# Kernel optimization log

Measured on AMD Instinct MI355X. Metric: run time of the kernel, lower is better.

The kernel has to match this reference:

```python
import jax, jax.numpy as jnp
import numpy as np


def _softsplat(tenIn, tenFlow):
    """Bilinear forward splatting: scatter tenIn to flow-displaced locations.
    tenIn: [N,C,H,W], tenFlow: [N,2,H,W] -> out [N,C,H,W]."""
    N, C, H, W = tenIn.shape
    dt = tenIn.dtype
    gx = jnp.arange(W, dtype=dt)[None, None, :]   # [1,1,W]
    gy = jnp.arange(H, dtype=dt)[None, :, None]   # [1,H,1]
    fx = gx + tenFlow[:, 0]                       # [N,H,W] target x
    fy = gy + tenFlow[:, 1]                       # [N,H,W] target y
    finite = jnp.isfinite(fx) & jnp.isfinite(fy)
    x0f = jnp.floor(fx)
    y0f = jnp.floor(fy)
    ix0 = x0f.astype(jnp.int32)
    iy0 = y0f.astype(jnp.int32)
    # bilinear corner weights (NW, NE, SW, SE) exactly as in the CUDA kernel
    wx1 = fx - x0f            # weight toward east
    wx0 = (x0f + 1.0) - fx    # weight toward west
    wy1 = fy - y0f            # weight toward south
    wy0 = (y0f + 1.0) - fy    # weight toward north
    corners = [
        (ix0,     iy0,     wx0 * wy0),  # NW
        (ix0 + 1, iy0,     wx1 * wy0),  # NE
        (ix0,     iy0 + 1, wx0 * wy1),  # SW
        (ix0 + 1, iy0 + 1, wx1 * wy1),  # SE
    ]
    HW = H * W
    tenIn_flat = tenIn.reshape(N, C, HW)

    def scatter_corner(ix, iy, w):
        valid = finite & (ix >= 0) & (ix < W) & (iy >= 0) & (iy < H)
        idx = jnp.where(valid, iy * W + ix, 0).reshape(N, HW)       # [N,HW]
        wv = jnp.where(valid, w, jnp.zeros_like(w)).reshape(N, 1, HW)
        vals = (tenIn_flat * wv).transpose(0, 2, 1)                 # [N,HW,C]
        seg = jax.vmap(lambda v, i: jax.ops.segment_sum(v, i, num_segments=HW))(vals, idx)
        return seg                                                   # [N,HW,C]

    out = scatter_corner(*corners[0])
    for c in corners[1:]:
        out = out + scatter_corner(*c)
    return out.transpose(0, 2, 1).reshape(N, C, H, W)


def softsplat_softmax(tenIn, tenFlow, tenMetric):
    # strMode == 'softmax': splat [tenIn * exp(metric), exp(metric)], then normalize
    w = jnp.exp(tenMetric)                          # [N,1,H,W]
    packed = jnp.concatenate([tenIn * w, w], axis=1)
    out = _softsplat(packed, tenFlow)
    norm = out[:, -1:]
    norm = jnp.where(norm == 0.0, jnp.ones_like(norm), norm)
    return out[:, :-1] / norm


def setup_inputs() -> dict:
    key = jax.random.key(0)
    k1, k2, k3 = jax.random.split(key, 3)
    N, C, H, W = 8, 64, 288, 512
    tenIn = jax.random.normal(k1, (N, C, H, W), dtype=jnp.float32)
    tenFlow = jax.random.normal(k2, (N, 2, H, W), dtype=jnp.float32)
    tenMetric = jax.random.normal(k3, (N, 1, H, W), dtype=jnp.float32)
    return {"tenIn": tenIn, "tenFlow": tenFlow, "tenMetric": tenMetric}


def reference(tenIn, tenFlow, tenMetric):
    return softsplat_softmax(tenIn, tenFlow, tenMetric)
```

## Files before the change

### kernel.cpp

```cpp
#include <hip/hip_runtime.h>
#include <hip/hip_fp16.h>
#include <math.h>

constexpr int N  = 8;
constexpr int C  = 64;
constexpr int H  = 288;
constexpr int W  = 512;
constexpr int HW = H * W;
constexpr int NPIX = N * HW;

constexpr int TW = 64, TH = 32, R = 8;
constexpr int PW = TW + 2 * R;
constexpr int PH = TH + 2 * R;
constexpr int PS = PW * PH;
constexpr int TGX = W / TW;
constexpr int TGY = H / TH;
constexpr int TILES = N * TGX * TGY;
constexpr int NOUT = TH * TW;
constexpr int K = 12;
constexpr int CCHB = 4;
constexpr int NCHUNK = C / CCHB;
constexpr int NSPLIT = 2;
constexpr int CPB = NCHUNK / NSPLIT;
constexpr int OVFCAP = 256;
constexpr int ESCCAP = 512;
constexpr int NTC = 512;
constexpr int NTG = 1024;
constexpr int GGRID = TILES * NSPLIT;

constexpr size_t CLAIM_LDS_WORDS = (size_t)NOUT * (K + 1);
constexpr size_t CLAIM_LDS_BYTES = CLAIM_LDS_WORDS * 4;

constexpr size_t WS_DEN  = 0;
constexpr size_t WS_META = WS_DEN  + (size_t)N * HW;
constexpr size_t WS_CNT  = WS_META + (size_t)TILES * NOUT * K;
constexpr size_t WS_OVFC = WS_CNT  + (size_t)TILES * NOUT;
constexpr size_t WS_OVFE = WS_OVFC + TILES;
constexpr size_t WS_ESCC = WS_OVFE + (size_t)TILES * OVFCAP * 2;
constexpr size_t WS_ESCE = WS_ESCC + TILES;

__device__ __forceinline__ int swz(int si) { return si ^ ((si >> 4) & 15); }

__device__ __forceinline__ unsigned packh2(float a, float b) {
    __half2 h = __floats2half2_rn(a, b);
    return *reinterpret_cast<unsigned*>(&h);
}
__device__ __forceinline__ float2 unpackh2(unsigned u) {
    __half2 h = *reinterpret_cast<__half2*>(&u);
    return __half22float2(h);
}

__global__ __launch_bounds__(NTC) void claim_kernel(
    const float* __restrict__ flow, const float* __restrict__ metric,
    unsigned* __restrict__ meta,
    unsigned* __restrict__ ovfc, unsigned* __restrict__ ovfe,
    float* __restrict__ den)
{
    extern __shared__ unsigned smem[];
    unsigned* cnt = smem;
    unsigned* ml  = smem + NOUT;

    for (int i = threadIdx.x; i < NOUT; i += NTC) cnt[i] = 0;
    for (int i = threadIdx.x; i < NOUT * K; i += NTC) ml[i] = 0u;
    __syncthreads();

    const int t  = blockIdx.x;
    const int n  = t / (TGX * TGY);
    const int r  = t % (TGX * TGY);
    const int Y0 = (r / TGX) * TH;
    const int X0 = (r % TGX) * TW;

    const float* fxp = flow + ((size_t)n * 2) * HW;
    const float* fyp = fxp + HW;
    const float* mp  = metric + (size_t)n * HW;
    unsigned* mt = meta + (size_t)t * NOUT * K;

    for (int si = threadIdx.x; si < PS; si += NTC) {
        int ys = Y0 - R + si / PW;
        int xs = X0 - R + si % PW;
        if ((unsigned)ys >= (unsigned)H || (unsigned)xs >= (unsigned)W) continue;
        int p = ys * W + xs;
        float fx = fxp[p] + (float)xs;
        float fy = fyp[p] + (float)ys;
        if (!(isfinite(fx) && isfinite(fy))) continue;
        float x0f = floorf(fx), y0f = floorf(fy);
        int tx = (int)x0f - X0;
        int ty = (int)y0f - Y0;
        float wx1 = fx - x0f, wx0 = x0f + 1.0f - fx;
        float wy1 = fy - y0f, wy0 = y0f + 1.0f - fy;
        float wm  = __expf(mp[p]);
        int sis = swz(si);

        #define CLAIM(TYv, TXv, Wv)                                           \
            if ((unsigned)(TYv) < (unsigned)TH &&                             \
                (unsigned)(TXv) < (unsigned)TW) {                             \
                float w_ = (Wv) * wm;                                         \
                int   o_ = (TYv) * TW + (TXv);                                \
                unsigned slot = atomicAdd(&cnt[o_], 1u);                      \
                if (slot < (unsigned)K) {                                     \
                    ml[o_ * K + (int)slot] =                                  \
                        ((unsigned)__half_as_ushort(__float2half(w_)) << 16)  \
                        | (unsigned)sis;                                      \
                } else {                                                      \
                    unsigned p2 = atomicAdd(&ovfc[t], 1u);                    \
                    if (p2 < (unsigned)OVFCAP) {                              \
                        unsigned* e = ovfe + ((size_t)t * OVFCAP + p2) * 2;   \
                        e[0] = ((unsigned)o_ << 16) | (unsigned)sis;          \
                        e[1] = __float_as_uint(w_);                           \
                    }                                                         \
                }                                                             \
            }
        CLAIM(ty,     tx,     wx0 * wy0)
        CLAIM(ty,     tx + 1, wx1 * wy0)
        CLAIM(ty + 1, tx,     wx0 * wy1)
        CLAIM(ty + 1, tx + 1, wx1 * wy1)
        #undef CLAIM
    }
    __syncthreads();

    const unsigned on = min(ovfc[t], (unsigned)OVFCAP);
    const unsigned* oe = ovfe + (size_t)t * OVFCAP * 2;
    for (int o = threadIdx.x; o < NOUT; o += NTC) {
        unsigned cn = min(cnt[o], (unsigned)K);
        float d = 0.0f;
        for (unsigned s = 0; s < cn; ++s)
            d += __half2float(__ushort_as_half(
                     (unsigned short)(ml[o * K + (int)s] >> 16)));
        for (unsigned i = 0; i < on; ++i)
            if ((oe[2 * i] >> 16) == (unsigned)o)
                d += __uint_as_float(oe[2 * i + 1]);
        den[(size_t)n * HW + (Y0 + o / TW) * W + X0 + o % TW] = d;
    }

    const uint4* mlv = reinterpret_cast<const uint4*>(ml);
    uint4* mtv = reinterpret_cast<uint4*>(mt);
    for (int i = threadIdx.x; i < NOUT * K / 4; i += NTC)
        mtv[i] = mlv[i];
}

__global__ __launch_bounds__(256) void escape_kernel(
    const float* __restrict__ flow, const float* __restrict__ metric,
    float* __restrict__ den, unsigned* __restrict__ escc,
    unsigned* __restrict__ esce)
{
    int pix = blockIdx.x * 256 + threadIdx.x;
    if (pix >= NPIX) return;
    int n  = pix / HW;
    int p  = pix - n * HW;
    int xs = p & (W - 1);
    int ys = p >> 9;

    float fx = flow[((size_t)n * 2    ) * HW + p] + (float)xs;
    float fy = flow[((size_t)n * 2 + 1) * HW + p] + (float)ys;
    if (!(isfinite(fx) && isfinite(fy))) return;
    float x0f = floorf(fx), y0f = floorf(fy);
    int ix0 = (int)x0f, iy0 = (int)y0f;
    float wx1 = fx - x0f, wx0 = x0f + 1.0f - fx;
    float wy1 = fy - y0f, wy0 = y0f + 1.0f - fy;

    int   cx[4] = { ix0, ix0 + 1, ix0,     ix0 + 1 };
    int   cy[4] = { iy0, iy0,     iy0 + 1, iy0 + 1 };
    float cw[4] = { wx0 * wy0, wx1 * wy0, wx0 * wy1, wx1 * wy1 };

    bool esc[4]; bool any = false;
    #pragma unroll
    for (int k = 0; k < 4; ++k) {
        esc[k] = false;
        if ((unsigned)cx[k] < (unsigned)W && (unsigned)cy[k] < (unsigned)H) {
            int tX0 = cx[k] & ~(TW - 1);
            int tY0 = cy[k] & ~(TH - 1);
            bool inpad = (xs >= tX0 - R) && (xs < tX0 + TW + R) &&
                         (ys >= tY0 - R) && (ys < tY0 + TH + R);
            if (!inpad) { esc[k] = true; any = true; }
        }
    }
    if (!any) return;

    float wm = __expf(metric[(size_t)n * HW + p]);
    #pragma unroll
    for (int k = 0; k < 4; ++k) {
        if (!esc[k]) continue;
        int tX0 = cx[k] & ~(TW - 1);
        int tY0 = cy[k] & ~(TH - 1);
        int tt  = n * (TGX * TGY) + (tY0 >> 5) * TGX + (tX0 >> 6);
        float w_ = cw[k] * wm;
        atomicAdd(den + (size_t)n * HW + cy[k] * W + cx[k], w_);
        unsigned pos = atomicAdd(&escc[tt], 1u);
        if (pos < (unsigned)ESCCAP) {
            unsigned* e = esce + ((size_t)tt * ESCCAP + pos) * 3;
            e[0] = (unsigned)((cy[k] - tY0) * TW + (cx[k] - tX0));
            e[1] = (unsigned)p;
            e[2] = __float_as_uint(w_);
        }
    }
}

__global__ __launch_bounds__(NTG, 4) void gather_kernel(
    const float* __restrict__ in, const unsigned* __restrict__ meta,
    const unsigned* __restrict__ ovfc,
    const unsigned* __restrict__ ovfe, const unsigned* __restrict__ escc,
    const unsigned* __restrict__ esce, const float* __restrict__ den,
    float* __restrict__ out)
{
    __shared__ uint2 val[2][PS];

    const int b0 = blockIdx.x;
    const int b  = (b0 & 7) * (GGRID / 8) + (b0 >> 3);
    const int t     = b >> 1;
    const int split = b & 1;
    const int n  = t / (TGX * TGY);
    const int r  = t % (TGX * TGY);
    const int Y0 = (r / TGX) * TH;
    const int X0 = (r % TGX) * TW;

    const unsigned on = min(ovfc[t], (unsigned)OVFCAP);
    const unsigned en = min(escc[t], (unsigned)ESCCAP);
    const unsigned* oe = ovfe + (size_t)t * OVFCAP * 2;
    const unsigned* ee = esce + (size_t)t * ESCCAP * 3;
    const unsigned* mt = meta + (size_t)t * NOUT * K;

    float inv[2];
    int   opix[2];
    #pragma unroll
    for (int k = 0; k < 2; ++k) {
        int o = threadIdx.x + k * NTG;
        opix[k] = (Y0 + o / TW) * W + X0 + o % TW;
        float d = den[(size_t)n * HW + opix[k]];
        inv[k] = (d == 0.0f) ? 1.0f : 1.0f / d;
    }

    const bool stager = threadIdx.x < PS / 4;
    int si0 = 0, sw = 0, soff = 0;
    bool ok = false;
    if (stager) {
        si0 = threadIdx.x * 4;
        int row = si0 / PW;
        int ys  = Y0 - R + row;
        int xs0 = X0 - R + (si0 - row * PW);
        ok  = (unsigned)ys < (unsigned)H && (unsigned)xs0 < (unsigned)W;
        sw  = (si0 >> 4) & 15;
        soff = ys * W + xs0;
    }
    const float* inb0 = in + ((size_t)n * C + split * CPB * CCHB) * HW;

    float4 g0 = {0,0,0,0}, g1 = g0, g2 = g0, g3 = g0;
    if (stager && ok) {
        const float* pp = inb0 + soff;
        g0 = *reinterpret_cast<const float4*>(pp);
        g1 = *reinterpret_cast<const float4*>(pp + HW);
        g2 = *reinterpret_cast<const float4*>(pp + 2 * HW);
        g3 = *reinterpret_cast<const float4*>(pp + 3 * HW);
    }
    if (stager) {
        val[0][(si0    ) ^ sw] = make_uint2(packh2(g0.x, g1.x), packh2(g2.x, g3.x));
        val[0][(si0 + 1) ^ sw] = make_uint2(packh2(g0.y, g1.y), packh2(g2.y, g3.y));
        val[0][(si0 + 2) ^ sw] = make_uint2(packh2(g0.z, g1.z), packh2(g2.z, g3.z));
        val[0][(si0 + 3) ^ sw] = make_uint2(packh2(g0.w, g1.w), packh2(g2.w, g3.w));
    }

    int cur = 0;
    for (int cc = 0; cc < CPB; ++cc) {
        __syncthreads();
        const float* inb = inb0 + (size_t)cc * CCHB * HW;

        if (cc + 1 < CPB && stager) {
            g0 = make_float4(0,0,0,0); g1 = g0; g2 = g0; g3 = g0;
            if (ok) {
                const float* pn = inb + (size_t)CCHB * HW + soff;
                g0 = *reinterpret_cast<const float4*>(pn);
                g1 = *reinterpret_cast<const float4*>(pn + HW);
                g2 = *reinterpret_cast<const float4*>(pn + 2 * HW);
                g3 = *reinterpret_cast<const float4*>(pn + 3 * HW);
            }
        }

        const uint2* vb = val[cur];
        #pragma unroll
        for (int k = 0; k < 2; ++k) {
            const int o = threadIdx.x + k * NTG;
            const uint4* mo4 = reinterpret_cast<const uint4*>(mt + (size_t)o * K);
            uint4 qa = mo4[0], qb = mo4[1], qc = mo4[2];
            unsigned mloc[K] = { qa.x, qa.y, qa.z, qa.w,
                                 qb.x, qb.y, qb.z, qb.w,
                                 qc.x, qc.y, qc.z, qc.w };

            float a0 = 0.0f, a1 = 0.0f, a2 = 0.0f, a3 = 0.0f;
            #pragma unroll
            for (int s = 0; s < K; ++s) {
                unsigned m_ = mloc[s];
                float w  = __half2float(__ushort_as_half((unsigned short)(m_ >> 16)));
                uint2 v = vb[m_ & 0xffffu];
                float2 f0 = unpackh2(v.x), f1 = unpackh2(v.y);
                a0 += w * f0.x;  a1 += w * f0.y;
                a2 += w * f1.x;  a3 += w * f1.y;
            }
            for (unsigned i = 0; i < on; ++i) {
                unsigned e0 = oe[2 * i];
                if ((e0 >> 16) == (unsigned)o) {
                    float w  = __uint_as_float(oe[2 * i + 1]);
                    uint2 v = vb[e0 & 0xffffu];
                    float2 f0 = unpackh2(v.x), f1 = unpackh2(v.y);
                    a0 += w * f0.x;  a1 += w * f0.y;
                    a2 += w * f1.x;  a3 += w * f1.y;
                }
            }
            for (unsigned i = 0; i < en; ++i) {
                if (ee[3 * i] == (unsigned)o) {
                    float w  = __uint_as_float(ee[3 * i + 2]);
                    int   ps = (int)ee[3 * i + 1];
                    a0 += w * inb[ps];
                    a1 += w * inb[ps + HW];
                    a2 += w * inb[ps + 2 * HW];
                    a3 += w * inb[ps + 3 * HW];
                }
            }
            size_t ob = ((size_t)n * C + (split * CPB + cc) * CCHB) * HW + opix[k];
            out[ob]          = a0 * inv[k];
            out[ob + HW]     = a1 * inv[k];
            out[ob + 2 * HW] = a2 * inv[k];
            out[ob + 3 * HW] = a3 * inv[k];
        }

        if (cc + 1 < CPB && stager) {
            uint2* vn = val[cur ^ 1];
            vn[(si0    ) ^ sw] = make_uint2(packh2(g0.x, g1.x), packh2(g2.x, g3.x));
            vn[(si0 + 1) ^ sw] = make_uint2(packh2(g0.y, g1.y), packh2(g2.y, g3.y));
            vn[(si0 + 2) ^ sw] = make_uint2(packh2(g0.z, g1.z), packh2(g2.z, g3.z));
            vn[(si0 + 3) ^ sw] = make_uint2(packh2(g0.w, g1.w), packh2(g2.w, g3.w));
        }
        cur ^= 1;
    }
}

extern "C" void kernel_launch(void* const* d_in, const int* in_sizes, int n_in,
                              void* d_out, int out_size, void* d_ws, size_t ws_size,
                              hipStream_t stream)
{
    const float* tenIn     = (const float*)d_in[0];
    const float* tenFlow   = (const float*)d_in[1];
    const float* tenMetric = (const float*)d_in[2];
    float* out = (float*)d_out;

    unsigned* ws  = (unsigned*)d_ws;
    float*    den = (float*)(ws + WS_DEN);
    unsigned* meta = ws + WS_META;
    unsigned* ovfc = ws + WS_OVFC;
    unsigned* ovfe = ws + WS_OVFE;
    unsigned* escc = ws + WS_ESCC;
    unsigned* esce = ws + WS_ESCE;

    hipFuncSetAttribute(reinterpret_cast<const void*>(claim_kernel),
                        hipFuncAttributeMaxDynamicSharedMemorySize,
                        (int)CLAIM_LDS_BYTES);

    hipMemsetAsync(ovfc, 0, TILES * sizeof(unsigned), stream);
    hipMemsetAsync(escc, 0, TILES * sizeof(unsigned), stream);

    claim_kernel<<<TILES, NTC, CLAIM_LDS_BYTES, stream>>>(tenFlow, tenMetric,
                                                          meta, ovfc, ovfe, den);
    escape_kernel<<<(NPIX + 255) / 256, 256, 0, stream>>>(tenFlow, tenMetric,
                                                          den, escc, esce);
    gather_kernel<<<GGRID, NTG, 0, stream>>>(tenIn, meta, ovfc,
                                             ovfe, escc, esce, den, out);
}
```

Before: 233.3 us.

## Fuse escape detection into claim kernel and shrink tiles to 32x32

Removes the separate escape kernel and has the claim kernel record escaping contributions for its own core pixels. Escaped weights are added to the denominator in the gather prologue instead of through global atomics. Tiles shrink to 32x32 and the channel split is dropped, so each gather block walks all channels with a cooperative double-buffered stage helper. The aim is to cut one full-image pass and the global atomics, at the cost of a larger halo-to-core ratio and a serial staging step inside the loop.

```diff
diff --git a/kernel.cpp b/kernel.cpp
--- a/kernel.cpp
+++ b/kernel.cpp
@@ -9,7 +9,7 @@
 constexpr int HW = H * W;
 constexpr int NPIX = N * HW;
 
-constexpr int TW = 64, TH = 32, R = 8;
+constexpr int TW = 32, TH = 32, R = 8;
 constexpr int PW = TW + 2 * R;
 constexpr int PH = TH + 2 * R;
 constexpr int PS = PW * PH;
@@ -20,21 +20,15 @@
 constexpr int K = 12;
 constexpr int CCHB = 4;
 constexpr int NCHUNK = C / CCHB;
-constexpr int NSPLIT = 2;
-constexpr int CPB = NCHUNK / NSPLIT;
 constexpr int OVFCAP = 256;
 constexpr int ESCCAP = 512;
 constexpr int NTC = 512;
-constexpr int NTG = 1024;
-constexpr int GGRID = TILES * NSPLIT;
-
-constexpr size_t CLAIM_LDS_WORDS = (size_t)NOUT * (K + 1);
-constexpr size_t CLAIM_LDS_BYTES = CLAIM_LDS_WORDS * 4;
+constexpr int NTG = 512;
+constexpr int TPX = TILES / 8;
 
 constexpr size_t WS_DEN  = 0;
 constexpr size_t WS_META = WS_DEN  + (size_t)N * HW;
-constexpr size_t WS_CNT  = WS_META + (size_t)TILES * NOUT * K;
-constexpr size_t WS_OVFC = WS_CNT  + (size_t)TILES * NOUT;
+constexpr size_t WS_OVFC = WS_META + (size_t)TILES * NOUT * K;
 constexpr size_t WS_OVFE = WS_OVFC + TILES;
 constexpr size_t WS_ESCC = WS_OVFE + (size_t)TILES * OVFCAP * 2;
 constexpr size_t WS_ESCE = WS_ESCC + TILES;
@@ -54,17 +48,18 @@
     const float* __restrict__ flow, const float* __restrict__ metric,
     unsigned* __restrict__ meta,
     unsigned* __restrict__ ovfc, unsigned* __restrict__ ovfe,
+    unsigned* __restrict__ escc, unsigned* __restrict__ esce,
     float* __restrict__ den)
 {
-    extern __shared__ unsigned smem[];
-    unsigned* cnt = smem;
-    unsigned* ml  = smem + NOUT;
+    __shared__ unsigned cnt[NOUT];
+    __shared__ unsigned ml[NOUT * K];
 
     for (int i = threadIdx.x; i < NOUT; i += NTC) cnt[i] = 0;
     for (int i = threadIdx.x; i < NOUT * K; i += NTC) ml[i] = 0u;
     __syncthreads();
 
-    const int t  = blockIdx.x;
+    const int b0 = blockIdx.x;
+    const int t  = (b0 & 7) * TPX + (b0 >> 3);
     const int n  = t / (TGX * TGY);
     const int r  = t % (TGX * TGY);
     const int Y0 = (r / TGX) * TH;
@@ -84,8 +79,9 @@
         float fy = fyp[p] + (float)ys;
         if (!(isfinite(fx) && isfinite(fy))) continue;
         float x0f = floorf(fx), y0f = floorf(fy);
-        int tx = (int)x0f - X0;
-        int ty = (int)y0f - Y0;
+        int ix0 = (int)x0f, iy0 = (int)y0f;
+        int tx = ix0 - X0;
+        int ty = iy0 - Y0;
         float wx1 = fx - x0f, wx0 = x0f + 1.0f - fx;
         float wy1 = fy - y0f, wy0 = y0f + 1.0f - fy;
         float wm  = __expf(mp[p]);
@@ -115,6 +111,31 @@
         CLAIM(ty + 1, tx,     wx0 * wy1)
         CLAIM(ty + 1, tx + 1, wx1 * wy1)
         #undef CLAIM
+
+        if ((unsigned)(xs - X0) < (unsigned)TW &&
+            (unsigned)(ys - Y0) < (unsigned)TH) {
+            int   cx[4] = { ix0, ix0 + 1, ix0,     ix0 + 1 };
+            int   cy[4] = { iy0, iy0,     iy0 + 1, iy0 + 1 };
+            float cw[4] = { wx0 * wy0, wx1 * wy0, wx0 * wy1, wx1 * wy1 };
+            #pragma unroll
+            for (int k = 0; k < 4; ++k) {
+                if ((unsigned)cx[k] >= (unsigned)W ||
+                    (unsigned)cy[k] >= (unsigned)H) continue;
+                int tX0 = cx[k] & ~(TW - 1);
+                int tY0 = cy[k] & ~(TH - 1);
+                bool inpad = (xs >= tX0 - R) && (xs < tX0 + TW + R) &&
+                             (ys >= tY0 - R) && (ys < tY0 + TH + R);
+                if (inpad) continue;
+                int tt = n * (TGX * TGY) + (tY0 >> 5) * TGX + (tX0 >> 5);
+                unsigned pos = atomicAdd(&escc[tt], 1u);
+                if (pos < (unsigned)ESCCAP) {
+                    unsigned* e = esce + ((size_t)tt * ESCCAP + pos) * 3;
+                    e[0] = (unsigned)((cy[k] - tY0) * TW + (cx[k] - tX0));
+                    e[1] = (unsigned)p;
+                    e[2] = __float_as_uint(cw[k] * wm);
+                }
+            }
+        }
     }
     __syncthreads();
 
@@ -138,80 +159,47 @@
         mtv[i] = mlv[i];
 }
 
-__global__ __launch_bounds__(256) void escape_kernel(
-    const float* __restrict__ flow, const float* __restrict__ metric,
-    float* __restrict__ den, unsigned* __restrict__ escc,
-    unsigned* __restrict__ esce)
+__device__ __forceinline__ void stage(
+    uint2* __restrict__ buf, const float* __restrict__ inb,
+    int X0, int Y0, int tid)
 {
-    int pix = blockIdx.x * 256 + threadIdx.x;
-    if (pix >= NPIX) return;
-    int n  = pix / HW;
-    int p  = pix - n * HW;
-    int xs = p & (W - 1);
-    int ys = p >> 9;
-
-    float fx = flow[((size_t)n * 2    ) * HW + p] + (float)xs;
-    float fy = flow[((size_t)n * 2 + 1) * HW + p] + (float)ys;
-    if (!(isfinite(fx) && isfinite(fy))) return;
-    float x0f = floorf(fx), y0f = floorf(fy);
-    int ix0 = (int)x0f, iy0 = (int)y0f;
-    float wx1 = fx - x0f, wx0 = x0f + 1.0f - fx;
-    float wy1 = fy - y0f, wy0 = y0f + 1.0f - fy;
-
-    int   cx[4] = { ix0, ix0 + 1, ix0,     ix0 + 1 };
-    int   cy[4] = { iy0, iy0,     iy0 + 1, iy0 + 1 };
-    float cw[4] = { wx0 * wy0, wx1 * wy0, wx0 * wy1, wx1 * wy1 };
-
-    bool esc[4]; bool any = false;
-    #pragma unroll
-    for (int k = 0; k < 4; ++k) {
-        esc[k] = false;
-        if ((unsigned)cx[k] < (unsigned)W && (unsigned)cy[k] < (unsigned)H) {
-            int tX0 = cx[k] & ~(TW - 1);
-            int tY0 = cy[k] & ~(TH - 1);
-            bool inpad = (xs >= tX0 - R) && (xs < tX0 + TW + R) &&
-                         (ys >= tY0 - R) && (ys < tY0 + TH + R);
-            if (!inpad) { esc[k] = true; any = true; }
+    for (int q = tid; q < PS / 4; q += NTG) {
+        int si0 = q * 4;
+        int row = si0 / PW;
+        int ys  = Y0 - R + row;
+        int xs0 = X0 - R + (si0 - row * PW);
+        bool ok = (unsigned)ys < (unsigned)H && (unsigned)xs0 < (unsigned)W;
+        float4 g0 = {0,0,0,0}, g1 = g0, g2 = g0, g3 = g0;
+        if (ok) {
+            const float* pp = inb + ys * W + xs0;
+            g0 = *reinterpret_cast<const float4*>(pp);
+            g1 = *reinterpret_cast<const float4*>(pp + HW);
+            g2 = *reinterpret_cast<const float4*>(pp + 2 * HW);
+            g3 = *reinterpret_cast<const float4*>(pp + 3 * HW);
         }
-    }
-    if (!any) return;
-
-    float wm = __expf(metric[(size_t)n * HW + p]);
-    #pragma unroll
-    for (int k = 0; k < 4; ++k) {
-        if (!esc[k]) continue;
-        int tX0 = cx[k] & ~(TW - 1);
-        int tY0 = cy[k] & ~(TH - 1);
-        int tt  = n * (TGX * TGY) + (tY0 >> 5) * TGX + (tX0 >> 6);
-        float w_ = cw[k] * wm;
-        atomicAdd(den + (size_t)n * HW + cy[k] * W + cx[k], w_);
-        unsigned pos = atomicAdd(&escc[tt], 1u);
-        if (pos < (unsigned)ESCCAP) {
-            unsigned* e = esce + ((size_t)tt * ESCCAP + pos) * 3;
-            e[0] = (unsigned)((cy[k] - tY0) * TW + (cx[k] - tX0));
-            e[1] = (unsigned)p;
-            e[2] = __float_as_uint(w_);
-        }
-    }
-}
-
-__global__ __launch_bounds__(NTG, 4) void gather_kernel(
+        int sw = (si0 >> 4) & 15;
+        buf[(si0    ) ^ sw] = make_uint2(packh2(g0.x, g1.x), packh2(g2.x, g3.x));
+        buf[(si0 + 1) ^ sw] = make_uint2(packh2(g0.y, g1.y), packh2(g2.y, g3.y));
+        buf[(si0 + 2) ^ sw] = make_uint2(packh2(g0.z, g1.z), packh2(g2.z, g3.z));
+        buf[(si0 + 3) ^ sw] = make_uint2(packh2(g0.w, g1.w), packh2(g2.w, g3.w));
+    }
+}
+
+__global__ __launch_bounds__(NTG, 8) void gather_kernel(
     const float* __restrict__ in, const unsigned* __restrict__ meta,
-    const unsigned* __restrict__ ovfc,
-    const unsigned* __restrict__ ovfe, const unsigned* __restrict__ escc,
-    const unsigned* __restrict__ esce, const float* __restrict__ den,
-    float* __restrict__ out)
+    const unsigned* __restrict__ ovfc, const unsigned* __restrict__ ovfe,
+    const unsigned* __restrict__ escc, const unsigned* __restrict__ esce,
+    const float* __restrict__ den, float* __restrict__ out)
 {
     __shared__ uint2 val[2][PS];
 
     const int b0 = blockIdx.x;
-    const int b  = (b0 & 7) * (GGRID / 8) + (b0 >> 3);
-    const int t     = b >> 1;
-    const int split = b & 1;
+    const int t  = (b0 & 7) * TPX + (b0 >> 3);
     const int n  = t / (TGX * TGY);
     const int r  = t % (TGX * TGY);
     const int Y0 = (r / TGX) * TH;
     const int X0 = (r % TGX) * TW;
+    const int tid = threadIdx.x;
 
     const unsigned on = min(ovfc[t], (unsigned)OVFCAP);
     const unsigned en = min(escc[t], (unsigned)ESCCAP);
@@ -223,61 +211,28 @@
     int   opix[2];
     #pragma unroll
     for (int k = 0; k < 2; ++k) {
-        int o = threadIdx.x + k * NTG;
+        int o = tid + k * NTG;
         opix[k] = (Y0 + o / TW) * W + X0 + o % TW;
         float d = den[(size_t)n * HW + opix[k]];
+        for (unsigned i = 0; i < en; ++i)
+            if (ee[3 * i] == (unsigned)o) d += __uint_as_float(ee[3 * i + 2]);
         inv[k] = (d == 0.0f) ? 1.0f : 1.0f / d;
     }
 
-    const bool stager = threadIdx.x < PS / 4;
-    int si0 = 0, sw = 0, soff = 0;
-    bool ok = false;
-    if (stager) {
-        si0 = threadIdx.x * 4;
-        int row = si0 / PW;
-        int ys  = Y0 - R + row;
-        int xs0 = X0 - R + (si0 - row * PW);
-        ok  = (unsigned)ys < (unsigned)H && (unsigned)xs0 < (unsigned)W;
-        sw  = (si0 >> 4) & 15;
-        soff = ys * W + xs0;
-    }
-    const float* inb0 = in + ((size_t)n * C + split * CPB * CCHB) * HW;
-
-    float4 g0 = {0,0,0,0}, g1 = g0, g2 = g0, g3 = g0;
-    if (stager && ok) {
-        const float* pp = inb0 + soff;
-        g0 = *reinterpret_cast<const float4*>(pp);
-        g1 = *reinterpret_cast<const float4*>(pp + HW);
-        g2 = *reinterpret_cast<const float4*>(pp + 2 * HW);
-        g3 = *reinterpret_cast<const float4*>(pp + 3 * HW);
-    }
-    if (stager) {
-        val[0][(si0    ) ^ sw] = make_uint2(packh2(g0.x, g1.x), packh2(g2.x, g3.x));
-        val[0][(si0 + 1) ^ sw] = make_uint2(packh2(g0.y, g1.y), packh2(g2.y, g3.y));
-        val[0][(si0 + 2) ^ sw] = make_uint2(packh2(g0.z, g1.z), packh2(g2.z, g3.z));
-        val[0][(si0 + 3) ^ sw] = make_uint2(packh2(g0.w, g1.w), packh2(g2.w, g3.w));
-    }
+    const float* inbase = in + (size_t)n * C * HW;
+    stage(val[0], inbase, X0, Y0, tid);
 
     int cur = 0;
-    for (int cc = 0; cc < CPB; ++cc) {
+    for (int cc = 0; cc < NCHUNK; ++cc) {
         __syncthreads();
-        const float* inb = inb0 + (size_t)cc * CCHB * HW;
-
-        if (cc + 1 < CPB && stager) {
-            g0 = make_float4(0,0,0,0); g1 = g0; g2 = g0; g3 = g0;
-            if (ok) {
-                const float* pn = inb + (size_t)CCHB * HW + soff;
-                g0 = *reinterpret_cast<const float4*>(pn);
-                g1 = *reinterpret_cast<const float4*>(pn + HW);
-                g2 = *reinterpret_cast<const float4*>(pn + 2 * HW);
-                g3 = *reinterpret_cast<const float4*>(pn + 3 * HW);
-            }
-        }
+        const float* inb = inbase + (size_t)cc * CCHB * HW;
+        if (cc + 1 < NCHUNK)
+            stage(val[cur ^ 1], inb + (size_t)CCHB * HW, X0, Y0, tid);
 
         const uint2* vb = val[cur];
         #pragma unroll
         for (int k = 0; k < 2; ++k) {
-            const int o = threadIdx.x + k * NTG;
+            const int o = tid + k * NTG;
             const uint4* mo4 = reinterpret_cast<const uint4*>(mt + (size_t)o * K);
             uint4 qa = mo4[0], qb = mo4[1], qc = mo4[2];
             unsigned mloc[K] = { qa.x, qa.y, qa.z, qa.w,
@@ -314,19 +269,11 @@
                     a3 += w * inb[ps + 3 * HW];
                 }
             }
-            size_t ob = ((size_t)n * C + (split * CPB + cc) * CCHB) * HW + opix[k];
+            size_t ob = ((size_t)n * C + cc * CCHB) * HW + opix[k];
             out[ob]          = a0 * inv[k];
             out[ob + HW]     = a1 * inv[k];
             out[ob + 2 * HW] = a2 * inv[k];
             out[ob + 3 * HW] = a3 * inv[k];
-        }
-
-        if (cc + 1 < CPB && stager) {
-            uint2* vn = val[cur ^ 1];
-            vn[(si0    ) ^ sw] = make_uint2(packh2(g0.x, g1.x), packh2(g2.x, g3.x));
-            vn[(si0 + 1) ^ sw] = make_uint2(packh2(g0.y, g1.y), packh2(g2.y, g3.y));
-            vn[(si0 + 2) ^ sw] = make_uint2(packh2(g0.z, g1.z), packh2(g2.z, g3.z));
-            vn[(si0 + 3) ^ sw] = make_uint2(packh2(g0.w, g1.w), packh2(g2.w, g3.w));
         }
         cur ^= 1;
     }
@@ -349,17 +296,11 @@
     unsigned* escc = ws + WS_ESCC;
     unsigned* esce = ws + WS_ESCE;
 
-    hipFuncSetAttribute(reinterpret_cast<const void*>(claim_kernel),
-                        hipFuncAttributeMaxDynamicSharedMemorySize,
-                        (int)CLAIM_LDS_BYTES);
-
     hipMemsetAsync(ovfc, 0, TILES * sizeof(unsigned), stream);
     hipMemsetAsync(escc, 0, TILES * sizeof(unsigned), stream);
 
-    claim_kernel<<<TILES, NTC, CLAIM_LDS_BYTES, stream>>>(tenFlow, tenMetric,
-                                                          meta, ovfc, ovfe, den);
-    escape_kernel<<<(NPIX + 255) / 256, 256, 0, stream>>>(tenFlow, tenMetric,
-                                                          den, escc, esce);
-    gather_kernel<<<GGRID, NTG, 0, stream>>>(tenIn, meta, ovfc,
-                                             ovfe, escc, esce, den, out);
-}
+    claim_kernel<<<TILES, NTC, 0, stream>>>(tenFlow, tenMetric, meta,
+                                            ovfc, ovfe, escc, esce, den);
+    gather_kernel<<<TILES, NTG, 0, stream>>>(tenIn, meta, ovfc, ovfe,
+                                             escc, esce, den, out);
+}
```

After: 569.2 us. 2.44x slower.

## Fold escape-list construction into claim kernel and drop separate escape pass

Applied to the files above, without the earlier changes.

Removes the standalone escape kernel, which re-read flow and metric for every pixel. The claim kernel now emits escape entries for its own interior pixels, and the gather kernel adds escape weights into the denominator by scanning the tile's escape list. This saves one launch and a full pass over flow, at the cost of extra branch work in claim and a per-output linear scan over escape entries in gather.

```diff
diff --git a/kernel.cpp b/kernel.cpp
--- a/kernel.cpp
+++ b/kernel.cpp
@@ -7,7 +7,6 @@
 constexpr int H  = 288;
 constexpr int W  = 512;
 constexpr int HW = H * W;
-constexpr int NPIX = N * HW;
 
 constexpr int TW = 64, TH = 32, R = 8;
 constexpr int PW = TW + 2 * R;
@@ -33,8 +32,7 @@
 
 constexpr size_t WS_DEN  = 0;
 constexpr size_t WS_META = WS_DEN  + (size_t)N * HW;
-constexpr size_t WS_CNT  = WS_META + (size_t)TILES * NOUT * K;
-constexpr size_t WS_OVFC = WS_CNT  + (size_t)TILES * NOUT;
+constexpr size_t WS_OVFC = WS_META + (size_t)TILES * NOUT * K;
 constexpr size_t WS_OVFE = WS_OVFC + TILES;
 constexpr size_t WS_ESCC = WS_OVFE + (size_t)TILES * OVFCAP * 2;
 constexpr size_t WS_ESCE = WS_ESCC + TILES;
@@ -54,6 +52,7 @@
     const float* __restrict__ flow, const float* __restrict__ metric,
     unsigned* __restrict__ meta,
     unsigned* __restrict__ ovfc, unsigned* __restrict__ ovfe,
+    unsigned* __restrict__ escc, unsigned* __restrict__ esce,
     float* __restrict__ den)
 {
     extern __shared__ unsigned smem[];
@@ -84,8 +83,9 @@
         float fy = fyp[p] + (float)ys;
         if (!(isfinite(fx) && isfinite(fy))) continue;
         float x0f = floorf(fx), y0f = floorf(fy);
-        int tx = (int)x0f - X0;
-        int ty = (int)y0f - Y0;
+        int ix0 = (int)x0f, iy0 = (int)y0f;
+        int tx = ix0 - X0;
+        int ty = iy0 - Y0;
         float wx1 = fx - x0f, wx0 = x0f + 1.0f - fx;
         float wy1 = fy - y0f, wy0 = y0f + 1.0f - fy;
         float wm  = __expf(mp[p]);
@@ -115,6 +115,31 @@
         CLAIM(ty + 1, tx,     wx0 * wy1)
         CLAIM(ty + 1, tx + 1, wx1 * wy1)
         #undef CLAIM
+
+        if ((unsigned)(xs - X0) < (unsigned)TW &&
+            (unsigned)(ys - Y0) < (unsigned)TH) {
+            int   cx[4] = { ix0, ix0 + 1, ix0,     ix0 + 1 };
+            int   cy[4] = { iy0, iy0,     iy0 + 1, iy0 + 1 };
+            float cw[4] = { wx0 * wy0, wx1 * wy0, wx0 * wy1, wx1 * wy1 };
+            #pragma unroll
+            for (int k = 0; k < 4; ++k) {
+                if ((unsigned)cx[k] >= (unsigned)W ||
+                    (unsigned)cy[k] >= (unsigned)H) continue;
+                int tX0 = cx[k] & ~(TW - 1);
+                int tY0 = cy[k] & ~(TH - 1);
+                bool inpad = (xs >= tX0 - R) && (xs < tX0 + TW + R) &&
+                             (ys >= tY0 - R) && (ys < tY0 + TH + R);
+                if (inpad) continue;
+                int tt = n * (TGX * TGY) + (tY0 >> 5) * TGX + (tX0 >> 6);
+                unsigned pos = atomicAdd(&escc[tt], 1u);
+                if (pos < (unsigned)ESCCAP) {
+                    unsigned* e = esce + ((size_t)tt * ESCCAP + pos) * 3;
+                    e[0] = (unsigned)((cy[k] - tY0) * TW + (cx[k] - tX0));
+                    e[1] = (unsigned)p;
+                    e[2] = __float_as_uint(cw[k] * wm);
+                }
+            }
+        }
     }
     __syncthreads();
 
@@ -138,69 +163,11 @@
         mtv[i] = mlv[i];
 }
 
-__global__ __launch_bounds__(256) void escape_kernel(
-    const float* __restrict__ flow, const float* __restrict__ metric,
-    float* __restrict__ den, unsigned* __restrict__ escc,
-    unsigned* __restrict__ esce)
-{
-    int pix = blockIdx.x * 256 + threadIdx.x;
-    if (pix >= NPIX) return;
-    int n  = pix / HW;
-    int p  = pix - n * HW;
-    int xs = p & (W - 1);
-    int ys = p >> 9;
-
-    float fx = flow[((size_t)n * 2    ) * HW + p] + (float)xs;
-    float fy = flow[((size_t)n * 2 + 1) * HW + p] + (float)ys;
-    if (!(isfinite(fx) && isfinite(fy))) return;
-    float x0f = floorf(fx), y0f = floorf(fy);
-    int ix0 = (int)x0f, iy0 = (int)y0f;
-    float wx1 = fx - x0f, wx0 = x0f + 1.0f - fx;
-    float wy1 = fy - y0f, wy0 = y0f + 1.0f - fy;
-
-    int   cx[4] = { ix0, ix0 + 1, ix0,     ix0 + 1 };
-    int   cy[4] = { iy0, iy0,     iy0 + 1, iy0 + 1 };
-    float cw[4] = { wx0 * wy0, wx1 * wy0, wx0 * wy1, wx1 * wy1 };
-
-    bool esc[4]; bool any = false;
-    #pragma unroll
-    for (int k = 0; k < 4; ++k) {
-        esc[k] = false;
-        if ((unsigned)cx[k] < (unsigned)W && (unsigned)cy[k] < (unsigned)H) {
-            int tX0 = cx[k] & ~(TW - 1);
-            int tY0 = cy[k] & ~(TH - 1);
-            bool inpad = (xs >= tX0 - R) && (xs < tX0 + TW + R) &&
-                         (ys >= tY0 - R) && (ys < tY0 + TH + R);
-            if (!inpad) { esc[k] = true; any = true; }
-        }
-    }
-    if (!any) return;
-
-    float wm = __expf(metric[(size_t)n * HW + p]);
-    #pragma unroll
-    for (int k = 0; k < 4; ++k) {
-        if (!esc[k]) continue;
-        int tX0 = cx[k] & ~(TW - 1);
-        int tY0 = cy[k] & ~(TH - 1);
-        int tt  = n * (TGX * TGY) + (tY0 >> 5) * TGX + (tX0 >> 6);
-        float w_ = cw[k] * wm;
-        atomicAdd(den + (size_t)n * HW + cy[k] * W + cx[k], w_);
-        unsigned pos = atomicAdd(&escc[tt], 1u);
-        if (pos < (unsigned)ESCCAP) {
-            unsigned* e = esce + ((size_t)tt * ESCCAP + pos) * 3;
-            e[0] = (unsigned)((cy[k] - tY0) * TW + (cx[k] - tX0));
-            e[1] = (unsigned)p;
-            e[2] = __float_as_uint(w_);
-        }
-    }
-}
-
 __global__ __launch_bounds__(NTG, 4) void gather_kernel(
     const float* __restrict__ in, const unsigned* __restrict__ meta,
-    const unsigned* __restrict__ ovfc,
-    const unsigned* __restrict__ ovfe, const unsigned* __restrict__ escc,
-    const unsigned* __restrict__ esce, const float* __restrict__ den,
-    float* __restrict__ out)
+    const unsigned* __restrict__ ovfc, const unsigned* __restrict__ ovfe,
+    const unsigned* __restrict__ escc, const unsigned* __restrict__ esce,
+    const float* __restrict__ den, float* __restrict__ out)
 {
     __shared__ uint2 val[2][PS];
 
@@ -226,6 +193,8 @@
         int o = threadIdx.x + k * NTG;
         opix[k] = (Y0 + o / TW) * W + X0 + o % TW;
         float d = den[(size_t)n * HW + opix[k]];
+        for (unsigned i = 0; i < en; ++i)
+            if (ee[3 * i] == (unsigned)o) d += __uint_as_float(ee[3 * i + 2]);
         inv[k] = (d == 0.0f) ? 1.0f : 1.0f / d;
     }
 
@@ -356,10 +325,8 @@
     hipMemsetAsync(ovfc, 0, TILES * sizeof(unsigned), stream);
     hipMemsetAsync(escc, 0, TILES * sizeof(unsigned), stream);
 
-    claim_kernel<<<TILES, NTC, CLAIM_LDS_BYTES, stream>>>(tenFlow, tenMetric,
-                                                          meta, ovfc, ovfe, den);
-    escape_kernel<<<(NPIX + 255) / 256, 256, 0, stream>>>(tenFlow, tenMetric,
-                                                          den, escc, esce);
-    gather_kernel<<<GGRID, NTG, 0, stream>>>(tenIn, meta, ovfc,
-                                             ovfe, escc, esce, den, out);
-}
+    claim_kernel<<<TILES, NTC, CLAIM_LDS_BYTES, stream>>>(
+        tenFlow, tenMetric, meta, ovfc, ovfe, escc, esce, den);
+    gather_kernel<<<GGRID, NTG, 0, stream>>>(tenIn, meta, ovfc, ovfe,
+                                             escc, esce, den, out);
+}
```

Measured after the change: 230.1 us (median of 2 runs). Within noise of the previous version (-1.4%).
